# Kernel optimization log

Hardware: AMD Instinct MI355X
Metric: run time of the kernel (lower is better)

## Reference

```python
import jax, jax.numpy as jnp
import numpy as np

DIM = 1024
N_HEADS = 16
HEAD_DIM = DIM // N_HEADS


def setup_inputs() -> dict:
    key = jax.random.key(0)
    ks = jax.random.split(key, 5)
    x = jax.random.normal(ks[0], (2, 2048, DIM), dtype=jnp.float32)
    # nn.Linear-style init scale
    s = 1.0 / np.sqrt(DIM)
    W_qkv = jax.random.uniform(ks[1], (DIM, 3 * DIM), jnp.float32, -s, s)
    b_qkv = jax.random.uniform(ks[2], (3 * DIM,), jnp.float32, -s, s)
    W_proj = jax.random.uniform(ks[3], (DIM, DIM), jnp.float32, -s, s)
    b_proj = jax.random.uniform(ks[4], (DIM,), jnp.float32, -s, s)
    return {"x": x, "W_qkv": W_qkv, "b_qkv": b_qkv, "W_proj": W_proj, "b_proj": b_proj}


def reference(x, W_qkv, b_qkv, W_proj, b_proj):
    B, S, D = x.shape
    scale = HEAD_DIM ** -0.5
    qkv = x @ W_qkv + b_qkv                                   # [B,S,3D]
    qkv = qkv.reshape(B, S, 3, N_HEADS, HEAD_DIM)
    q = qkv[:, :, 0].transpose(0, 2, 1, 3)                    # [B,H,S,d]
    k = qkv[:, :, 1].transpose(0, 2, 1, 3)
    v = qkv[:, :, 2].transpose(0, 2, 1, 3)
    attn = jnp.einsum('bhqd,bhkd->bhqk', q, k) * scale        # [B,H,S,S]
    attn = jax.nn.softmax(attn, axis=-1)
    out = jnp.einsum('bhqk,bhkd->bhqd', attn, v)              # [B,H,S,d]
    out = out.transpose(0, 2, 1, 3).reshape(B, S, D)
    return out @ W_proj + b_proj
```

## Files before the change

kernel.cpp:

```cpp
#include <hip/hip_runtime.h>
#include <stdint.h>

typedef unsigned short u16;
typedef __attribute__((ext_vector_type(8))) short bf16x8;
typedef __attribute__((ext_vector_type(4))) float f32x4;
typedef __attribute__((ext_vector_type(4))) u16 us4;
typedef __attribute__((ext_vector_type(8))) u16 us8;

__device__ __forceinline__ u16 f2bf(float f) {
  union { float f; unsigned u; } v; v.f = f;
  unsigned r = v.u + 0x7fffu + ((v.u >> 16) & 1u);
  return (u16)(r >> 16);
}

__device__ __forceinline__ unsigned pkbf(float a, float b) {
  union { float f; unsigned u; } x, y; x.f = a; y.f = b;
  return __builtin_amdgcn_perm(y.u + 0x8000u, x.u + 0x8000u, 0x07060302u);
}

__device__ __forceinline__ float fast_exp2(float x) {
#if __has_builtin(__builtin_amdgcn_exp2f)
  return __builtin_amdgcn_exp2f(x);
#else
  return exp2f(x);
#endif
}

__device__ __forceinline__ void gld16(const void* g, void* l) {
  __builtin_amdgcn_global_load_lds(
      (const __attribute__((address_space(1))) void*)g,
      (__attribute__((address_space(3))) void*)l, 16, 0, 0);
}

__global__ void cvt_kernel(const float* __restrict__ in, u16* __restrict__ out, int n4) {
  int i = blockIdx.x * blockDim.x + threadIdx.x;
  if (i >= n4) return;
  f32x4 v = ((const f32x4*)in)[i];
  us4 r;
#pragma unroll
  for (int j = 0; j < 4; ++j) r[j] = f2bf(v[j]);
  ((us4*)out)[i] = r;
}

__global__ void transw_kernel(const float* __restrict__ in, u16* __restrict__ out, int R, int C) {
  __shared__ u16 tile[32][33];
  const int tx = threadIdx.x & 31, ty = threadIdx.x >> 5;
  const int c0 = blockIdx.x * 32, r0 = blockIdx.y * 32;
#pragma unroll
  for (int j = 0; j < 4; ++j)
    tile[ty + j * 8][tx] = f2bf(in[(size_t)(r0 + ty + j * 8) * C + c0 + tx]);
  __syncthreads();
#pragma unroll
  for (int j = 0; j < 4; ++j)
    out[(size_t)(c0 + ty + j * 8) * R + r0 + tx] = tile[tx][ty + j * 8];
}

__global__ __launch_bounds__(256) void qkv_gemm_kernel(
    const u16* __restrict__ A, const u16* __restrict__ Bt, const float* __restrict__ bias,
    u16* __restrict__ Qb, u16* __restrict__ Kb, u16* __restrict__ Vtb) {
  __shared__ u16 sm[17408];
  u16* As = sm;
  u16* Bs = sm + 4096;
  const int tid = threadIdx.x;
  const int w = tid >> 6, l = tid & 63, quad = l >> 4, lanelo = l & 15;
  const int wr = w >> 1, wc = w & 1;
  const long m0 = (long)blockIdx.x * 128;
  const long n0 = (long)blockIdx.y * 128;

  f32x4 acc[4][4];
#pragma unroll
  for (int i = 0; i < 4; ++i)
#pragma unroll
    for (int j = 0; j < 4; ++j) acc[i][j] = (f32x4){0.f, 0.f, 0.f, 0.f};

  const u16* ag = A + (m0 + w * 32 + (l >> 2)) * 1024 + (l & 3) * 8;
  const u16* bg = Bt + (n0 + w * 32 + (l >> 2)) * 1024 + (l & 3) * 8;
  u16* asl = As + w * 1024;
  u16* bsl = Bs + w * 1024;

  for (int kt = 0; kt < 32; ++kt) {
    const int ko = kt * 32;
    gld16(ag + ko, asl);
    gld16(ag + 16 * 1024 + ko, asl + 512);
    gld16(bg + ko, bsl);
    gld16(bg + 16 * 1024 + ko, bsl + 512);
    __syncthreads();
    bf16x8 af[4], bf[4];
#pragma unroll
    for (int mt = 0; mt < 4; ++mt)
      af[mt] = *(const bf16x8*)(As + (wr * 64 + mt * 16 + lanelo) * 32 + quad * 8);
#pragma unroll
    for (int nt = 0; nt < 4; ++nt)
      bf[nt] = *(const bf16x8*)(Bs + (wc * 64 + nt * 16 + lanelo) * 32 + quad * 8);
#pragma unroll
    for (int mt = 0; mt < 4; ++mt)
#pragma unroll
      for (int nt = 0; nt < 4; ++nt)
        acc[mt][nt] = __builtin_amdgcn_mfma_f32_16x16x32_bf16(af[mt], bf[nt], acc[mt][nt], 0, 0, 0);
    __syncthreads();
  }

  const int t = (int)(n0 >> 10);
  const float scl = (t == 0) ? 0.18033688011112042f : 1.0f;

  float bias_v[4];
#pragma unroll
  for (int nt = 0; nt < 4; ++nt) bias_v[nt] = bias[n0 + wc * 64 + nt * 16 + lanelo];

  u16* Ct = sm;
#pragma unroll
  for (int mt = 0; mt < 4; ++mt)
#pragma unroll
    for (int nt = 0; nt < 4; ++nt)
#pragma unroll
      for (int r = 0; r < 4; ++r)
        Ct[(wr * 64 + mt * 16 + quad * 4 + r) * 136 + wc * 64 + nt * 16 + lanelo] =
            f2bf((acc[mt][nt][r] + bias_v[nt]) * scl);
  __syncthreads();

  const int b = (int)(m0 >> 11);
  const int s0 = (int)(m0 & 2047);
  const int h0 = (int)((n0 & 1023) >> 6);

  if (t < 2) {
    u16* dst = (t == 0) ? Qb : Kb;
#pragma unroll
    for (int p = 0; p < 8; ++p) {
      const int hh = p >> 2;
      const int sl = (p & 3) * 32 + (tid >> 3);
      const int c8 = tid & 7;
      us8 v = *(const us8*)(Ct + sl * 136 + hh * 64 + c8 * 8);
      const int pos = (c8 + sl) & 7;
      const size_t off = ((size_t)((b * 16 + h0 + hh) * 2048 + s0 + sl)) * 64 + pos * 8;
      *(us8*)(dst + off) = v;
    }
  } else {
#pragma unroll
    for (int p = 0; p < 8; ++p) {
      const int hh = p >> 2;
      const int dl = (p & 3) * 16 + (tid >> 4);
      const int c16 = tid & 15;
      us8 v;
#pragma unroll
      for (int j = 0; j < 8; ++j) v[j] = Ct[(c16 * 8 + j) * 136 + hh * 64 + dl];
      const int pos = (c16 + dl) & 15;
      const size_t off = ((size_t)((b * 16 + h0 + hh) * 64 + dl)) * 2048 + s0 + pos * 8;
      *(us8*)(Vtb + off) = v;
    }
  }
}

__global__ __launch_bounds__(256) void attn_kernel(
    const u16* __restrict__ Qb, const u16* __restrict__ Kb,
    const u16* __restrict__ Vtb, u16* __restrict__ Ob) {
  __shared__ u16 Ks[128 * 64];
  __shared__ u16 Vs[64 * 128];
  __shared__ u16 Ps[4][32 * 64];
  const int tid = threadIdx.x;
  const int w = tid >> 6, l = tid & 63, quad = l >> 4, lanelo = l & 15;
  const int qt = blockIdx.x, head = blockIdx.y;
  const int b = head >> 4, h = head & 15;
  const u16* Qh = Qb + (size_t)head * 2048 * 64;
  const u16* Kh = Kb + (size_t)head * 2048 * 64;
  const u16* Vh = Vtb + (size_t)head * 64 * 2048;
  u16* Pw = &Ps[w][0];

  bf16x8 qf[2][2];
#pragma unroll
  for (int mt = 0; mt < 2; ++mt)
#pragma unroll
    for (int ks = 0; ks < 2; ++ks) {
      const int row = qt * 128 + w * 32 + mt * 16 + lanelo;
      const int pos = (ks * 4 + quad + lanelo) & 7;
      qf[mt][ks] = *(const bf16x8*)(Qh + (size_t)row * 64 + pos * 8);
    }

  f32x4 o[2][4], os[2];
#pragma unroll
  for (int mt = 0; mt < 2; ++mt) {
    os[mt] = (f32x4){0.f, 0.f, 0.f, 0.f};
#pragma unroll
    for (int ot = 0; ot < 4; ++ot) o[mt][ot] = (f32x4){0.f, 0.f, 0.f, 0.f};
  }
  bf16x8 ones;
#pragma unroll
  for (int j = 0; j < 8; ++j) ones[j] = (short)0x3F80;

  for (int kt = 0; kt < 16; ++kt) {
    const u16* kbase = Kh + kt * 8192;
#pragma unroll
    for (int j = 0; j < 4; ++j) {
      const int i = w * 4 + j;
      gld16(kbase + i * 512 + l * 8, &Ks[i * 512]);
    }
#pragma unroll
    for (int j = 0; j < 4; ++j) {
      const int i = w * 4 + j;
      const int dd = i * 4 + (l >> 4);
      gld16(Vh + (size_t)dd * 2048 + kt * 128 + (l & 15) * 8, &Vs[i * 512]);
    }
    __syncthreads();

    f32x4 s[2][8];
#pragma unroll
    for (int mt = 0; mt < 2; ++mt)
#pragma unroll
      for (int nt = 0; nt < 8; ++nt) s[mt][nt] = (f32x4){0.f, 0.f, 0.f, 0.f};

#pragma unroll
    for (int ks = 0; ks < 2; ++ks) {
#pragma unroll
      for (int nt = 0; nt < 8; ++nt) {
        const int keyl = nt * 16 + lanelo;
        const int pos = (ks * 4 + quad + lanelo) & 7;
        bf16x8 kf = *(const bf16x8*)(&Ks[keyl * 64 + pos * 8]);
        s[0][nt] = __builtin_amdgcn_mfma_f32_16x16x32_bf16(kf, qf[0][ks], s[0][nt], 0, 0, 0);
        s[1][nt] = __builtin_amdgcn_mfma_f32_16x16x32_bf16(kf, qf[1][ks], s[1][nt], 0, 0, 0);
      }
    }

#pragma unroll
    for (int half = 0; half < 2; ++half) {
#pragma unroll
      for (int mt = 0; mt < 2; ++mt)
#pragma unroll
        for (int nt4 = 0; nt4 < 4; ++nt4) {
          f32x4 sv = s[mt][half * 4 + nt4];
          const float p0 = fast_exp2(sv[0]), p1 = fast_exp2(sv[1]);
          const float p2 = fast_exp2(sv[2]), p3 = fast_exp2(sv[3]);
          uint2 pk;
          pk.x = pkbf(p0, p1);
          pk.y = pkbf(p2, p3);
          const int row = mt * 16 + lanelo;
          const int chunk = nt4 * 2 + (quad >> 1);
          const int pos = (chunk + lanelo) & 7;
          *(uint2*)(&Pw[row * 64 + pos * 8 + (quad & 1) * 4]) = pk;
        }

#pragma unroll
      for (int ks2 = 0; ks2 < 2; ++ks2) {
        bf16x8 pf[2];
#pragma unroll
        for (int mt = 0; mt < 2; ++mt) {
          const int row = mt * 16 + lanelo;
          const int pos = (ks2 * 4 + quad + lanelo) & 7;
          pf[mt] = *(const bf16x8*)(&Pw[row * 64 + pos * 8]);
        }
        os[0] = __builtin_amdgcn_mfma_f32_16x16x32_bf16(pf[0], ones, os[0], 0, 0, 0);
        os[1] = __builtin_amdgcn_mfma_f32_16x16x32_bf16(pf[1], ones, os[1], 0, 0, 0);
        const int ksg = half * 2 + ks2;
#pragma unroll
        for (int ot = 0; ot < 4; ++ot) {
          const int dim = ot * 16 + lanelo;
          const int pos = (ksg * 4 + quad + lanelo) & 15;
          bf16x8 vf = *(const bf16x8*)(&Vs[dim * 128 + pos * 8]);
          o[0][ot] = __builtin_amdgcn_mfma_f32_16x16x32_bf16(pf[0], vf, o[0][ot], 0, 0, 0);
          o[1][ot] = __builtin_amdgcn_mfma_f32_16x16x32_bf16(pf[1], vf, o[1][ot], 0, 0, 0);
        }
      }
    }
    __syncthreads();
  }

#pragma unroll
  for (int mt = 0; mt < 2; ++mt)
#pragma unroll
    for (int r = 0; r < 4; ++r) {
      const float inv = 1.0f / os[mt][r];
      const int srow = qt * 128 + w * 32 + mt * 16 + quad * 4 + r;
      const size_t base = ((size_t)(b * 2048 + srow)) * 1024 + h * 64;
#pragma unroll
      for (int ot = 0; ot < 4; ++ot)
        Ob[base + ot * 16 + lanelo] = f2bf(o[mt][ot][r] * inv);
    }
}

__global__ __launch_bounds__(256) void proj_gemm_kernel(
    const u16* __restrict__ A, const u16* __restrict__ Bt,
    const float* __restrict__ bias, float* __restrict__ out) {
  __shared__ u16 sm[8192];
  u16* As = sm;
  u16* Bs = sm + 4096;
  const int tid = threadIdx.x;
  const int w = tid >> 6, l = tid & 63, quad = l >> 4, lanelo = l & 15;
  const int wr = w >> 1, wc = w & 1;
  const long m0 = (long)blockIdx.x * 128;
  const long n0 = (long)blockIdx.y * 128;

  f32x4 acc[4][4];
#pragma unroll
  for (int i = 0; i < 4; ++i)
#pragma unroll
    for (int j = 0; j < 4; ++j) acc[i][j] = (f32x4){0.f, 0.f, 0.f, 0.f};

  const u16* ag = A + (m0 + w * 32 + (l >> 2)) * 1024 + (l & 3) * 8;
  const u16* bg = Bt + (n0 + w * 32 + (l >> 2)) * 1024 + (l & 3) * 8;
  u16* asl = As + w * 1024;
  u16* bsl = Bs + w * 1024;

  for (int kt = 0; kt < 32; ++kt) {
    const int ko = kt * 32;
    gld16(ag + ko, asl);
    gld16(ag + 16 * 1024 + ko, asl + 512);
    gld16(bg + ko, bsl);
    gld16(bg + 16 * 1024 + ko, bsl + 512);
    __syncthreads();
    bf16x8 af[4], bf[4];
#pragma unroll
    for (int mt = 0; mt < 4; ++mt)
      af[mt] = *(const bf16x8*)(As + (wr * 64 + mt * 16 + lanelo) * 32 + quad * 8);
#pragma unroll
    for (int nt = 0; nt < 4; ++nt)
      bf[nt] = *(const bf16x8*)(Bs + (wc * 64 + nt * 16 + lanelo) * 32 + quad * 8);
#pragma unroll
    for (int mt = 0; mt < 4; ++mt)
#pragma unroll
      for (int nt = 0; nt < 4; ++nt)
        acc[mt][nt] = __builtin_amdgcn_mfma_f32_16x16x32_bf16(af[mt], bf[nt], acc[mt][nt], 0, 0, 0);
    __syncthreads();
  }

  float bias_v[4];
#pragma unroll
  for (int nt = 0; nt < 4; ++nt) bias_v[nt] = bias[n0 + wc * 64 + nt * 16 + lanelo];

#pragma unroll
  for (int mt = 0; mt < 4; ++mt)
#pragma unroll
    for (int nt = 0; nt < 4; ++nt)
#pragma unroll
      for (int r = 0; r < 4; ++r) {
        const size_t m = m0 + wr * 64 + mt * 16 + quad * 4 + r;
        const size_t n = n0 + wc * 64 + nt * 16 + lanelo;
        out[m * 1024 + n] = acc[mt][nt][r] + bias_v[nt];
      }
}

extern "C" void kernel_launch(void* const* d_in, const int* in_sizes, int n_in,
                              void* d_out, int out_size, void* d_ws, size_t ws_size,
                              hipStream_t stream) {
  const float* x = (const float*)d_in[0];
  const float* Wqkv = (const float*)d_in[1];
  const float* bqkv = (const float*)d_in[2];
  const float* Wproj = (const float*)d_in[3];
  const float* bproj = (const float*)d_in[4];
  float* out = (float*)d_out;
  char* ws = (char*)d_ws;

  u16* Xb   = (u16*)(ws);
  u16* Ob   = (u16*)(ws);
  u16* Wqkt = (u16*)(ws + 8388608);
  u16* Wpt  = (u16*)(ws + 14680064);
  u16* Qb   = (u16*)(ws + 16777216);
  u16* Kb   = (u16*)(ws + 25165824);
  u16* Vtb  = (u16*)(ws + 33554432);

  cvt_kernel<<<4096, 256, 0, stream>>>(x, Xb, 1048576);
  transw_kernel<<<dim3(96, 32), 256, 0, stream>>>(Wqkv, Wqkt, 1024, 3072);
  transw_kernel<<<dim3(32, 32), 256, 0, stream>>>(Wproj, Wpt, 1024, 1024);
  qkv_gemm_kernel<<<dim3(32, 24), 256, 0, stream>>>(Xb, Wqkt, bqkv, Qb, Kb, Vtb);
  attn_kernel<<<dim3(16, 32), 256, 0, stream>>>(Qb, Kb, Vtb, Ob);
  proj_gemm_kernel<<<dim3(32, 8), 256, 0, stream>>>(Ob, Wpt, bproj, out);
}
```

Before: 195.0 us.

## Split attention and projection over key/K halves with 32x32 MFMA and combine pass

```diff
diff --git a/kernel.cpp b/kernel.cpp
--- a/kernel.cpp
+++ b/kernel.cpp
@@ -4,6 +4,7 @@
 typedef unsigned short u16;
 typedef __attribute__((ext_vector_type(8))) short bf16x8;
 typedef __attribute__((ext_vector_type(4))) float f32x4;
+typedef __attribute__((ext_vector_type(16))) float f32x16;
 typedef __attribute__((ext_vector_type(4))) u16 us4;
 typedef __attribute__((ext_vector_type(8))) u16 us8;
 
@@ -11,6 +12,11 @@
   union { float f; unsigned u; } v; v.f = f;
   unsigned r = v.u + 0x7fffu + ((v.u >> 16) & 1u);
   return (u16)(r >> 16);
+}
+
+__device__ __forceinline__ float bf2f(u16 b) {
+  union { float f; unsigned u; } v; v.u = ((unsigned)b) << 16;
+  return v.f;
 }
 
 __device__ __forceinline__ unsigned pkbf(float a, float b) {
@@ -150,44 +156,37 @@
   }
 }
 
-__global__ __launch_bounds__(256) void attn_kernel(
+__global__ __launch_bounds__(256, 4) void attn_kernel(
     const u16* __restrict__ Qb, const u16* __restrict__ Kb,
-    const u16* __restrict__ Vtb, u16* __restrict__ Ob) {
-  __shared__ u16 Ks[128 * 64];
-  __shared__ u16 Vs[64 * 128];
-  __shared__ u16 Ps[4][32 * 64];
+    const u16* __restrict__ Vtb, u16* __restrict__ Op, float* __restrict__ lp) {
+  __shared__ u16 Ks[8192];
+  __shared__ u16 Vs[8192];
   const int tid = threadIdx.x;
-  const int w = tid >> 6, l = tid & 63, quad = l >> 4, lanelo = l & 15;
-  const int qt = blockIdx.x, head = blockIdx.y;
-  const int b = head >> 4, h = head & 15;
+  const int w = tid >> 6, l = tid & 63;
+  const int m = l & 31, hi = l >> 5;
+  const int qt = blockIdx.x, head = blockIdx.y, z = blockIdx.z;
   const u16* Qh = Qb + (size_t)head * 2048 * 64;
   const u16* Kh = Kb + (size_t)head * 2048 * 64;
   const u16* Vh = Vtb + (size_t)head * 64 * 2048;
-  u16* Pw = &Ps[w][0];
-
-  bf16x8 qf[2][2];
-#pragma unroll
-  for (int mt = 0; mt < 2; ++mt)
-#pragma unroll
-    for (int ks = 0; ks < 2; ++ks) {
-      const int row = qt * 128 + w * 32 + mt * 16 + lanelo;
-      const int pos = (ks * 4 + quad + lanelo) & 7;
-      qf[mt][ks] = *(const bf16x8*)(Qh + (size_t)row * 64 + pos * 8);
-    }
-
-  f32x4 o[2][4], os[2];
-#pragma unroll
-  for (int mt = 0; mt < 2; ++mt) {
-    os[mt] = (f32x4){0.f, 0.f, 0.f, 0.f};
-#pragma unroll
-    for (int ot = 0; ot < 4; ++ot) o[mt][ot] = (f32x4){0.f, 0.f, 0.f, 0.f};
-  }
-  bf16x8 ones;
-#pragma unroll
-  for (int j = 0; j < 8; ++j) ones[j] = (short)0x3F80;
-
-  for (int kt = 0; kt < 16; ++kt) {
-    const u16* kbase = Kh + kt * 8192;
+  const int permaddr = (l ^ 32) << 2;
+
+  const int qrow = qt * 128 + w * 32 + m;
+  bf16x8 qf[4];
+#pragma unroll
+  for (int ks = 0; ks < 4; ++ks) {
+    const int c = ks * 2 + hi;
+    const int pos = (c + qrow) & 7;
+    qf[ks] = *(const bf16x8*)(Qh + (size_t)qrow * 64 + pos * 8);
+  }
+
+  f32x16 o0, o1;
+#pragma unroll
+  for (int i = 0; i < 16; ++i) { o0[i] = 0.f; o1[i] = 0.f; }
+  float sacc = 0.f;
+
+  for (int kt = 0; kt < 8; ++kt) {
+    const int kb = z * 8 + kt;
+    const u16* kbase = Kh + (size_t)kb * 8192;
 #pragma unroll
     for (int j = 0; j < 4; ++j) {
       const int i = w * 4 + j;
@@ -197,82 +196,98 @@
     for (int j = 0; j < 4; ++j) {
       const int i = w * 4 + j;
       const int dd = i * 4 + (l >> 4);
-      gld16(Vh + (size_t)dd * 2048 + kt * 128 + (l & 15) * 8, &Vs[i * 512]);
-    }
-    __syncthreads();
-
-    f32x4 s[2][8];
-#pragma unroll
-    for (int mt = 0; mt < 2; ++mt)
-#pragma unroll
-      for (int nt = 0; nt < 8; ++nt) s[mt][nt] = (f32x4){0.f, 0.f, 0.f, 0.f};
-
-#pragma unroll
-    for (int ks = 0; ks < 2; ++ks) {
-#pragma unroll
-      for (int nt = 0; nt < 8; ++nt) {
-        const int keyl = nt * 16 + lanelo;
-        const int pos = (ks * 4 + quad + lanelo) & 7;
-        bf16x8 kf = *(const bf16x8*)(&Ks[keyl * 64 + pos * 8]);
-        s[0][nt] = __builtin_amdgcn_mfma_f32_16x16x32_bf16(kf, qf[0][ks], s[0][nt], 0, 0, 0);
-        s[1][nt] = __builtin_amdgcn_mfma_f32_16x16x32_bf16(kf, qf[1][ks], s[1][nt], 0, 0, 0);
+      gld16(Vh + (size_t)dd * 2048 + kb * 128 + (l & 15) * 8, &Vs[i * 512]);
+    }
+    __syncthreads();
+
+#pragma unroll
+    for (int g = 0; g < 4; ++g) {
+      f32x16 st;
+#pragma unroll
+      for (int i = 0; i < 16; ++i) st[i] = 0.f;
+      const int key = g * 32 + m;
+#pragma unroll
+      for (int ks = 0; ks < 4; ++ks) {
+        const int c = ks * 2 + hi;
+        const int pos = (c + key) & 7;
+        bf16x8 kf = *(const bf16x8*)(&Ks[key * 64 + pos * 8]);
+        st = __builtin_amdgcn_mfma_f32_32x32x16_bf16(kf, qf[ks], st, 0, 0, 0);
       }
-    }
-
-#pragma unroll
-    for (int half = 0; half < 2; ++half) {
-#pragma unroll
-      for (int mt = 0; mt < 2; ++mt)
-#pragma unroll
-        for (int nt4 = 0; nt4 < 4; ++nt4) {
-          f32x4 sv = s[mt][half * 4 + nt4];
-          const float p0 = fast_exp2(sv[0]), p1 = fast_exp2(sv[1]);
-          const float p2 = fast_exp2(sv[2]), p3 = fast_exp2(sv[3]);
-          uint2 pk;
-          pk.x = pkbf(p0, p1);
-          pk.y = pkbf(p2, p3);
-          const int row = mt * 16 + lanelo;
-          const int chunk = nt4 * 2 + (quad >> 1);
-          const int pos = (chunk + lanelo) & 7;
-          *(uint2*)(&Pw[row * 64 + pos * 8 + (quad & 1) * 4]) = pk;
-        }
-
-#pragma unroll
-      for (int ks2 = 0; ks2 < 2; ++ks2) {
-        bf16x8 pf[2];
-#pragma unroll
-        for (int mt = 0; mt < 2; ++mt) {
-          const int row = mt * 16 + lanelo;
-          const int pos = (ks2 * 4 + quad + lanelo) & 7;
-          pf[mt] = *(const bf16x8*)(&Pw[row * 64 + pos * 8]);
-        }
-        os[0] = __builtin_amdgcn_mfma_f32_16x16x32_bf16(pf[0], ones, os[0], 0, 0, 0);
-        os[1] = __builtin_amdgcn_mfma_f32_16x16x32_bf16(pf[1], ones, os[1], 0, 0, 0);
-        const int ksg = half * 2 + ks2;
-#pragma unroll
-        for (int ot = 0; ot < 4; ++ot) {
-          const int dim = ot * 16 + lanelo;
-          const int pos = (ksg * 4 + quad + lanelo) & 15;
-          bf16x8 vf = *(const bf16x8*)(&Vs[dim * 128 + pos * 8]);
-          o[0][ot] = __builtin_amdgcn_mfma_f32_16x16x32_bf16(pf[0], vf, o[0][ot], 0, 0, 0);
-          o[1][ot] = __builtin_amdgcn_mfma_f32_16x16x32_bf16(pf[1], vf, o[1][ot], 0, 0, 0);
+
+      float p[16];
+#pragma unroll
+      for (int r = 0; r < 16; ++r) p[r] = fast_exp2(st[r]);
+#pragma unroll
+      for (int r = 0; r < 16; ++r) sacc += p[r];
+
+      unsigned L[8];
+#pragma unroll
+      for (int q4 = 0; q4 < 4; ++q4) {
+        L[2 * q4] = pkbf(p[4 * q4], p[4 * q4 + 1]);
+        L[2 * q4 + 1] = pkbf(p[4 * q4 + 2], p[4 * q4 + 3]);
+      }
+
+#pragma unroll
+      for (int s = 0; s < 2; ++s) {
+        const unsigned a0 = L[4 * s], a1 = L[4 * s + 1];
+        const unsigned b0 = L[4 * s + 2], b1 = L[4 * s + 3];
+        const unsigned s0 = hi ? a0 : b0;
+        const unsigned s1 = hi ? a1 : b1;
+        const unsigned r0 = (unsigned)__builtin_amdgcn_ds_bpermute(permaddr, (int)s0);
+        const unsigned r1 = (unsigned)__builtin_amdgcn_ds_bpermute(permaddr, (int)s1);
+        int4 fd;
+        fd.x = (int)(hi ? r0 : a0);
+        fd.y = (int)(hi ? r1 : a1);
+        fd.z = (int)(hi ? b0 : r0);
+        fd.w = (int)(hi ? b1 : r1);
+        union { int4 i; bf16x8 v; } pu; pu.i = fd;
+        const int c = g * 4 + s * 2 + hi;
+#pragma unroll
+        for (int n = 0; n < 2; ++n) {
+          const int d = n * 32 + m;
+          const int pos = (c + d) & 15;
+          bf16x8 vf = *(const bf16x8*)(&Vs[d * 128 + pos * 8]);
+          if (n == 0) o0 = __builtin_amdgcn_mfma_f32_32x32x16_bf16(pu.v, vf, o0, 0, 0, 0);
+          else        o1 = __builtin_amdgcn_mfma_f32_32x32x16_bf16(pu.v, vf, o1, 0, 0, 0);
         }
       }
     }
     __syncthreads();
   }
 
-#pragma unroll
-  for (int mt = 0; mt < 2; ++mt)
-#pragma unroll
-    for (int r = 0; r < 4; ++r) {
-      const float inv = 1.0f / os[mt][r];
-      const int srow = qt * 128 + w * 32 + mt * 16 + quad * 4 + r;
-      const size_t base = ((size_t)(b * 2048 + srow)) * 1024 + h * 64;
-#pragma unroll
-      for (int ot = 0; ot < 4; ++ot)
-        Ob[base + ot * 16 + lanelo] = f2bf(o[mt][ot][r] * inv);
-    }
+  union { float f; int i; } sv; sv.f = sacc;
+  union { float f; int i; } pv; pv.i = __builtin_amdgcn_ds_bpermute(permaddr, sv.i);
+  const float ltot = sacc + pv.f;
+  if (hi == 0)
+    lp[(size_t)z * 65536 + (size_t)head * 2048 + qt * 128 + w * 32 + m] = ltot;
+
+  const int b = head >> 4, h = head & 15;
+  u16* Od = Op + (size_t)z * 4194304;
+#pragma unroll
+  for (int r = 0; r < 16; ++r) {
+    const int qlocal = (r & 3) + 8 * (r >> 2) + 4 * hi;
+    const size_t base =
+        ((size_t)(b * 2048 + qt * 128 + w * 32 + qlocal)) * 1024 + h * 64;
+    Od[base + m] = f2bf(o0[r]);
+    Od[base + 32 + m] = f2bf(o1[r]);
+  }
+}
+
+__global__ __launch_bounds__(128) void combine_kernel(
+    const u16* __restrict__ Op, const float* __restrict__ lp, u16* __restrict__ Ob) {
+  const int r = blockIdx.x;
+  const int tid = threadIdx.x;
+  const int col = tid * 8;
+  const int b = r >> 11, s = r & 2047, h = col >> 6;
+  const size_t li = (size_t)(b * 16 + h) * 2048 + s;
+  const float linv = 1.0f / (lp[li] + lp[65536 + li]);
+  us8 v0 = *(const us8*)(Op + (size_t)r * 1024 + col);
+  us8 v1 = *(const us8*)(Op + 4194304 + (size_t)r * 1024 + col);
+  us8 o;
+#pragma unroll
+  for (int j = 0; j < 8; ++j)
+    o[j] = f2bf((bf2f(v0[j]) + bf2f(v1[j])) * linv);
+  *(us8*)(Ob + (size_t)r * 1024 + col) = o;
 }
 
 __global__ __launch_bounds__(256) void proj_gemm_kernel(
@@ -286,6 +301,7 @@
   const int wr = w >> 1, wc = w & 1;
   const long m0 = (long)blockIdx.x * 128;
   const long n0 = (long)blockIdx.y * 128;
+  const int z = blockIdx.z;
 
   f32x4 acc[4][4];
 #pragma unroll
@@ -293,12 +309,12 @@
 #pragma unroll
     for (int j = 0; j < 4; ++j) acc[i][j] = (f32x4){0.f, 0.f, 0.f, 0.f};
 
-  const u16* ag = A + (m0 + w * 32 + (l >> 2)) * 1024 + (l & 3) * 8;
-  const u16* bg = Bt + (n0 + w * 32 + (l >> 2)) * 1024 + (l & 3) * 8;
+  const u16* ag = A + (m0 + w * 32 + (l >> 2)) * 1024 + z * 512 + (l & 3) * 8;
+  const u16* bg = Bt + (n0 + w * 32 + (l >> 2)) * 1024 + z * 512 + (l & 3) * 8;
   u16* asl = As + w * 1024;
   u16* bsl = Bs + w * 1024;
 
-  for (int kt = 0; kt < 32; ++kt) {
+  for (int kt = 0; kt < 16; ++kt) {
     const int ko = kt * 32;
     gld16(ag + ko, asl);
     gld16(ag + 16 * 1024 + ko, asl + 512);
@@ -322,7 +338,8 @@
 
   float bias_v[4];
 #pragma unroll
-  for (int nt = 0; nt < 4; ++nt) bias_v[nt] = bias[n0 + wc * 64 + nt * 16 + lanelo];
+  for (int nt = 0; nt < 4; ++nt)
+    bias_v[nt] = z ? 0.f : bias[n0 + wc * 64 + nt * 16 + lanelo];
 
 #pragma unroll
   for (int mt = 0; mt < 4; ++mt)
@@ -330,9 +347,9 @@
     for (int nt = 0; nt < 4; ++nt)
 #pragma unroll
       for (int r = 0; r < 4; ++r) {
-        const size_t m = m0 + wr * 64 + mt * 16 + quad * 4 + r;
-        const size_t n = n0 + wc * 64 + nt * 16 + lanelo;
-        out[m * 1024 + n] = acc[mt][nt][r] + bias_v[nt];
+        const size_t mm = m0 + wr * 64 + mt * 16 + quad * 4 + r;
+        const size_t nn = n0 + wc * 64 + nt * 16 + lanelo;
+        atomicAdd(&out[mm * 1024 + nn], acc[mt][nt][r] + bias_v[nt]);
       }
 }
 
@@ -348,17 +365,22 @@
   char* ws = (char*)d_ws;
 
   u16* Xb   = (u16*)(ws);
-  u16* Ob   = (u16*)(ws);
+  u16* Op   = (u16*)(ws);
   u16* Wqkt = (u16*)(ws + 8388608);
-  u16* Wpt  = (u16*)(ws + 14680064);
   u16* Qb   = (u16*)(ws + 16777216);
+  u16* Ob   = (u16*)(ws + 16777216);
   u16* Kb   = (u16*)(ws + 25165824);
   u16* Vtb  = (u16*)(ws + 33554432);
+  u16* Wpt  = (u16*)(ws + 41943040);
+  float* lp = (float*)(ws + 44040192);
+
+  hipMemsetAsync(out, 0, (size_t)4096 * 1024 * 4, stream);
 
   cvt_kernel<<<4096, 256, 0, stream>>>(x, Xb, 1048576);
   transw_kernel<<<dim3(96, 32), 256, 0, stream>>>(Wqkv, Wqkt, 1024, 3072);
   transw_kernel<<<dim3(32, 32), 256, 0, stream>>>(Wproj, Wpt, 1024, 1024);
   qkv_gemm_kernel<<<dim3(32, 24), 256, 0, stream>>>(Xb, Wqkt, bqkv, Qb, Kb, Vtb);
-  attn_kernel<<<dim3(16, 32), 256, 0, stream>>>(Qb, Kb, Vtb, Ob);
-  proj_gemm_kernel<<<dim3(32, 8), 256, 0, stream>>>(Ob, Wpt, bproj, out);
-}
+  attn_kernel<<<dim3(16, 32, 2), 256, 0, stream>>>(Qb, Kb, Vtb, Op, lp);
+  combine_kernel<<<4096, 128, 0, stream>>>(Op, lp, Ob);
+  proj_gemm_kernel<<<dim3(32, 8, 2), 256, 0, stream>>>(Ob, Wpt, bproj, out);
+}
```

After: 218.7 us. +12.2%, slower.
